# Kernel tuning notes

Hardware: AMD Instinct MI355X
Metric: run time of the kernel (lower is better)

The kernel has to match this reference:

```python
import jax, jax.numpy as jnp
import numpy as np

B = 128
NHEAD = 16
D_MODEL = 512
D_IN = 256  # each of f_* and f_*_out; concat -> 512
N_ATOM = 128


def _scopes():
    lens = np.array([96 + (i % 33) for i in range(B)], dtype=np.int64)  # max == 128 == N_ATOM
    starts_a = np.concatenate([[1], 1 + np.cumsum(lens)[:-1]]).astype(np.int64)
    nb = 2 * lens
    starts_b = np.concatenate([[1], 1 + np.cumsum(nb)[:-1]]).astype(np.int64)
    return lens, starts_a, nb, starts_b


def setup_inputs() -> dict:
    key = jax.random.key(0)
    ks = jax.random.split(key, 10)
    lens, starts_a, nb, starts_b = _scopes()
    Na = int(1 + lens.sum())   # 14279 (row 0 is padding)
    Nb = int(1 + nb.sum())     # 28557 (bond 0 is padding)
    f_atoms = jax.random.normal(ks[0], (Na, D_IN), jnp.float32)
    f_bonds = jax.random.normal(ks[1], (Nb, D_IN), jnp.float32)
    f_atoms_out = jax.random.normal(ks[2], (Na, D_IN), jnp.float32)
    f_bonds_out = jax.random.normal(ks[3], (Nb, D_IN), jnp.float32)
    b2a = jax.random.randint(ks[4], (Nb,), 0, 96, jnp.int64 if jax.config.jax_enable_x64 else jnp.int32)
    b2revb = jax.random.randint(ks[5], (Nb,), 0, Nb, b2a.dtype)
    a_scope = jnp.stack([jnp.asarray(starts_a), jnp.asarray(lens)], axis=1)
    b_scope = jnp.stack([jnp.asarray(starts_b), jnp.asarray(nb)], axis=1)
    W_atom = jax.random.normal(ks[6], (2 * D_IN, D_MODEL), jnp.float32) * 0.02
    b_atom = jnp.zeros((D_MODEL,), jnp.float32)
    W_bond = jax.random.normal(ks[7], (2 * D_IN, NHEAD), jnp.float32) * 0.02
    b_bond = jnp.zeros((NHEAD,), jnp.float32)
    return {"f_atoms": f_atoms, "f_bonds": f_bonds, "f_atoms_out": f_atoms_out,
            "f_bonds_out": f_bonds_out, "b2a": b2a, "b2revb": b2revb,
            "a_scope": a_scope, "b_scope": b_scope, "n_atom": N_ATOM,
            "W_atom": W_atom, "b_atom": b_atom, "W_bond": W_bond, "b_bond": b_bond}


def reference(f_atoms, f_bonds, f_atoms_out, f_bonds_out, b2a, b2revb,
              a_scope, b_scope, n_atom, W_atom, b_atom, W_bond, b_bond):
    Bsz = a_scope.shape[0]
    # atom embedding: concat + linear, drop padding row 0, pad per-molecule -> [n_atom, B, d]
    atoms = jnp.concatenate([f_atoms, f_atoms_out], axis=1) @ W_atom + b_atom  # [Na, d]
    starts_a, lens_a = a_scope[:, 0], a_scope[:, 1]
    pos = jnp.arange(n_atom)
    valid = pos[None, :] < lens_a[:, None]                       # [B, n_atom]
    gidx = jnp.where(valid, starts_a[:, None] + pos[None, :], 0)  # safe gather idx
    atoms_pad = jnp.where(valid[..., None], atoms[gidx], 0.0)     # [B, n_atom, d]
    atoms_emb = atoms_pad.transpose(1, 0, 2)                      # [n_atom, B, d] (batch_first=False)
    # bond embedding -> scatter into dense pairwise matrix
    bonds = jnp.concatenate([f_bonds, f_bonds_out], axis=1) @ W_bond + b_bond  # [Nb, nhead]
    Nb = bonds.shape[0]
    starts_b = b_scope[:, 0]
    mol = jnp.searchsorted(starts_b, jnp.arange(Nb), side='right') - 1  # molecule id per bond (-1 for pad bond 0)
    offset = jnp.maximum(mol, 0) * (n_atom * n_atom)
    idx = b2a + b2a[b2revb] * n_atom + offset                     # flat index into [B*n_atom*n_atom]
    flat = jnp.zeros((Bsz * n_atom * n_atom, bonds.shape[1]), bonds.dtype).at[idx].set(bonds)
    apairs = flat.reshape(Bsz, n_atom, n_atom, -1)                # [B, n_atom, n_atom, nhead]
    padding_mask = ~valid                                         # [B, n_atom], True = pad
    apairs = jnp.where(padding_mask[:, None, :, None], -jnp.inf, apairs)
    apairs = apairs.transpose(0, 3, 1, 2)                         # [B, nhead, n_atom, n_atom]
    return atoms_emb, apairs, padding_mask
```

## Files before the change

### kernel.cpp

```cpp
#include <hip/hip_runtime.h>
#include <math.h>

#define NEG_BIG (-1e30f)

typedef __attribute__((ext_vector_type(8))) short short8;
typedef __attribute__((ext_vector_type(8))) _Float16 half8;
typedef __attribute__((ext_vector_type(4))) float floatx4;

__device__ __forceinline__ unsigned short f2bf(float x) {
    unsigned u = __float_as_uint(x);
    unsigned r = (u + 0x7fffu + ((u >> 16) & 1u)) >> 16;
    return (unsigned short)r;
}
__device__ __forceinline__ short f2h(float x) {
    _Float16 h = (_Float16)x;
    return __builtin_bit_cast(short, h);
}
__device__ __forceinline__ float h2f(short s) {
    return (float)__builtin_bit_cast(_Float16, s);
}


__device__ __forceinline__ void bonds_body(
    int bbid, char* smem,
    const float* __restrict__ fB, const float* __restrict__ fBo,
    const float* __restrict__ Wb_raw, const float* __restrict__ bb_,
    float* __restrict__ bonds, int Nb)
{
    short* feat = (short*)smem;
    short* wb   = (short*)(smem + 17408);

    const int tid = threadIdx.x;
    const int j0 = bbid * 64;

    for (int c = tid; c < 8192; c += 256) {
        int k = c >> 4, h = c & 15;
        wb[h * 512 + ((((k >> 3) + h) & 63) << 3) + (k & 7)] = (short)f2bf(Wb_raw[c]);
    }

    const int wid = tid >> 6, lane = tid & 63;
    const int quad = lane >> 4, l16 = lane & 15;
    floatx4 acc = (floatx4){0.f, 0.f, 0.f, 0.f};

    const int fr = tid >> 2;
    const int fs = (tid & 3) * 32;
    const int j = j0 + fr;

    for (int k0 = 0; k0 < 512; k0 += 128) {
        float x[32];
        if (j < Nb) {
            const float* p = (k0 < 256) ? (fB + (size_t)j * 256 + k0 + fs)
                                        : (fBo + (size_t)j * 256 + (k0 - 256) + fs);
#pragma unroll
            for (int i = 0; i < 8; i++) {
                float4 v = ((const float4*)p)[i];
                x[i * 4 + 0] = v.x; x[i * 4 + 1] = v.y;
                x[i * 4 + 2] = v.z; x[i * 4 + 3] = v.w;
            }
        } else {
#pragma unroll
            for (int i = 0; i < 32; i++) x[i] = 0.f;
        }
        __syncthreads();
#pragma unroll
        for (int c = 0; c < 4; c++) {
            short8 s;
#pragma unroll
            for (int i = 0; i < 8; i++) s[i] = (short)f2bf(x[c * 8 + i]);
            *(short8*)&feat[fr * 136 + fs + c * 8] = s;
        }
        __syncthreads();
#pragma unroll
        for (int kk = 0; kk < 4; kk++) {
            short8 a = *(const short8*)&feat[(wid * 16 + l16) * 136 + kk * 32 + quad * 8];
            int kchunk = (k0 + kk * 32 + quad * 8) >> 3;
            short8 b = *(const short8*)&wb[l16 * 512 + (((kchunk + l16) & 63) * 8)];
            acc = __builtin_amdgcn_mfma_f32_16x16x32_bf16(a, b, acc, 0, 0, 0);
        }
    }
    float bv = bb_[l16];
#pragma unroll
    for (int r = 0; r < 4; r++) {
        int jj = j0 + wid * 16 + quad * 4 + r;
        if (jj < Nb) bonds[(size_t)jj * 16 + l16] = acc[r] + bv;
    }
}

__device__ __forceinline__ void scatter_body(
    int sbid, char* smem,
    const int* __restrict__ b2a, const int* __restrict__ b2revb,
    const int* __restrict__ b_scope, int* __restrict__ winner,
    int Nb, int Bmol)
{
    int* sb = (int*)smem;
    int tid = threadIdx.x;
    if (tid < Bmol) sb[tid] = b_scope[2 * tid];
    __syncthreads();
    int j = sbid * 256 + tid;
    if (j >= Nb) return;
    int lo = 0, hi = Bmol;
    while (lo < hi) { int mid = (lo + hi) >> 1; if (sb[mid] <= j) lo = mid + 1; else hi = mid; }
    int mol = lo - 1; if (mol < 0) mol = 0;
    int p2 = b2a[j];
    int p1 = b2a[b2revb[j]];
    atomicMax(&winner[mol * 16384 + p1 * 128 + p2], j);
}

__device__ __forceinline__ void atoms_body(
    int abid, char* smem,
    const float* __restrict__ fA, const float* __restrict__ fAo,
    const int* __restrict__ a_scope,
    const short* __restrict__ WH, const short* __restrict__ WL,
    const float* __restrict__ bias, float* __restrict__ out, int Bmol)
{
    short* A_s = (short*)smem;
    short* B_s = (short*)(smem + 20480);
    int*   rs  = (int*)(smem + 40960);

    const int tid = threadIdx.x;
    const int n0 = (abid & 3) * 128;
    const int mol = abid >> 2;

    if (tid < 128) {
        int len = a_scope[2 * mol + 1];
        rs[tid] = (tid < len) ? (a_scope[2 * mol] + tid) : -1;
    }
    const int wid = tid >> 6, lane = tid & 63;
    const int wm = (wid >> 1) * 64, wn = (wid & 1) * 64;
    const int quad = lane >> 4, l16 = lane & 15;

    floatx4 acc1[4][4], acc2[4][4];
#pragma unroll
    for (int i = 0; i < 4; i++)
#pragma unroll
        for (int j = 0; j < 4; j++) {
            acc1[i][j] = (floatx4){0.f, 0.f, 0.f, 0.f};
            acc2[i][j] = (floatx4){0.f, 0.f, 0.f, 0.f};
        }

    const int ar = tid >> 1;
    const int ak = (tid & 1) * 16;
    __syncthreads();
    const int asrc = rs[ar];

    for (int k0 = 0; k0 < 512; k0 += 32) {
        float x[16];
        if (asrc >= 0) {
            int kg = k0 + ak;
            const float* p = (kg < 256) ? (fA + (size_t)asrc * 256 + kg)
                                        : (fAo + (size_t)asrc * 256 + (kg - 256));
#pragma unroll
            for (int i = 0; i < 4; i++) {
                float4 v = ((const float4*)p)[i];
                x[i * 4 + 0] = v.x; x[i * 4 + 1] = v.y;
                x[i * 4 + 2] = v.z; x[i * 4 + 3] = v.w;
            }
        } else {
#pragma unroll
            for (int i = 0; i < 16; i++) x[i] = 0.f;
        }
        size_t goff = (size_t)(n0 + ar) * 512 + k0 + ak;
        short8 bh0 = *(const short8*)(WH + goff);
        short8 bh1 = *(const short8*)(WH + goff + 8);
        short8 bl0 = *(const short8*)(WL + goff);
        short8 bl1 = *(const short8*)(WL + goff + 8);

        short8 ah0, ah1, al0, al1;
#pragma unroll
        for (int i = 0; i < 8; i++) {
            short h = f2h(x[i]);
            float r = (x[i] - h2f(h)) * 2048.0f;
            ah0[i] = h; al0[i] = f2h(r);
        }
#pragma unroll
        for (int i = 0; i < 8; i++) {
            float xx = x[8 + i];
            short h = f2h(xx);
            float r = (xx - h2f(h)) * 2048.0f;
            ah1[i] = h; al1[i] = f2h(r);
        }

        __syncthreads();
        const int abase = ar * 40 + ak;
        *(short8*)&A_s[abase] = ah0;          *(short8*)&A_s[abase + 8] = ah1;
        *(short8*)&A_s[5120 + abase] = al0;   *(short8*)&A_s[5120 + abase + 8] = al1;
        *(short8*)&B_s[abase] = bh0;          *(short8*)&B_s[abase + 8] = bh1;
        *(short8*)&B_s[5120 + abase] = bl0;   *(short8*)&B_s[5120 + abase + 8] = bl1;
        __syncthreads();

        half8 afh[4], afl[4];
#pragma unroll
        for (int ti = 0; ti < 4; ti++) {
            int off = (wm + ti * 16 + l16) * 40 + quad * 8;
            afh[ti] = *(const half8*)&A_s[off];
            afl[ti] = *(const half8*)&A_s[5120 + off];
        }
#pragma unroll
        for (int tj = 0; tj < 4; tj++) {
            int off = (wn + tj * 16 + l16) * 40 + quad * 8;
            half8 bh = *(const half8*)&B_s[off];
            half8 bl = *(const half8*)&B_s[5120 + off];
#pragma unroll
            for (int ti = 0; ti < 4; ti++) {
                acc1[ti][tj] = __builtin_amdgcn_mfma_f32_16x16x32_f16(afh[ti], bh, acc1[ti][tj], 0, 0, 0);
                acc2[ti][tj] = __builtin_amdgcn_mfma_f32_16x16x32_f16(afh[ti], bl, acc2[ti][tj], 0, 0, 0);
                acc2[ti][tj] = __builtin_amdgcn_mfma_f32_16x16x32_f16(afl[ti], bh, acc2[ti][tj], 0, 0, 0);
            }
        }
    }

#pragma unroll
    for (int tj = 0; tj < 4; tj++) {
        int n = n0 + wn + tj * 16 + l16;
        float bv = bias[n];
#pragma unroll
        for (int ti = 0; ti < 4; ti++) {
#pragma unroll
            for (int r = 0; r < 4; r++) {
                int pos = wm + ti * 16 + quad * 4 + r;
                bool valid = rs[pos] >= 0;
                float v = valid ? (acc1[ti][tj][r] + 4.8828125e-4f * acc2[ti][tj][r] + bv) : 0.f;
                out[((size_t)pos * Bmol + mol) * 512 + n] = v;
            }
        }
    }
}

__device__ __forceinline__ void apairs_body(
    int chunk, const int* __restrict__ winner, const float* __restrict__ bonds,
    const int* __restrict__ a_scope, float* __restrict__ out_ap)
{
    int t = chunk * 256 + threadIdx.x;
    int b = t >> 12;
    int p1 = (t >> 5) & 127;
    int p2q = t & 31;
    int len = a_scope[2 * b + 1];
    const int4 w = ((const int4*)winner)[t];

    int wi0 = w.x, wi1 = w.y, wi2 = w.z, wi3 = w.w;
    float rows[4][16];
#pragma unroll
    for (int c = 0; c < 16; c++) {
        rows[0][c] = 0.f; rows[1][c] = 0.f; rows[2][c] = 0.f; rows[3][c] = 0.f;
    }
    if (wi0 >= 0) {
        const float4* p = (const float4*)(bonds + (size_t)wi0 * 16);
#pragma unroll
        for (int c = 0; c < 4; c++) {
            float4 v = p[c];
            rows[0][4*c+0] = v.x; rows[0][4*c+1] = v.y; rows[0][4*c+2] = v.z; rows[0][4*c+3] = v.w;
        }
    }
    if (wi1 >= 0) {
        const float4* p = (const float4*)(bonds + (size_t)wi1 * 16);
#pragma unroll
        for (int c = 0; c < 4; c++) {
            float4 v = p[c];
            rows[1][4*c+0] = v.x; rows[1][4*c+1] = v.y; rows[1][4*c+2] = v.z; rows[1][4*c+3] = v.w;
        }
    }
    if (wi2 >= 0) {
        const float4* p = (const float4*)(bonds + (size_t)wi2 * 16);
#pragma unroll
        for (int c = 0; c < 4; c++) {
            float4 v = p[c];
            rows[2][4*c+0] = v.x; rows[2][4*c+1] = v.y; rows[2][4*c+2] = v.z; rows[2][4*c+3] = v.w;
        }
    }
    if (wi3 >= 0) {
        const float4* p = (const float4*)(bonds + (size_t)wi3 * 16);
#pragma unroll
        for (int c = 0; c < 4; c++) {
            float4 v = p[c];
            rows[3][4*c+0] = v.x; rows[3][4*c+1] = v.y; rows[3][4*c+2] = v.z; rows[3][4*c+3] = v.w;
        }
    }

    bool iv0 = (p2q * 4 + 0 >= len);
    bool iv1 = (p2q * 4 + 1 >= len);
    bool iv2 = (p2q * 4 + 2 >= len);
    bool iv3 = (p2q * 4 + 3 >= len);
    float* ob = out_ap + ((size_t)b * 16 * 128 + p1) * 128 + p2q * 4;
#pragma unroll
    for (int h = 0; h < 16; h++) {
        float4 v;
        v.x = iv0 ? NEG_BIG : rows[0][h];
        v.y = iv1 ? NEG_BIG : rows[1][h];
        v.z = iv2 ? NEG_BIG : rows[2][h];
        v.w = iv3 ? NEG_BIG : rows[3][h];
        *(float4*)(ob + (size_t)h * 16384) = v;
    }
}

__global__ __launch_bounds__(256) void k_phase1(
    const float* __restrict__ fB, const float* __restrict__ fBo,
    const float* __restrict__ Wb_raw, const float* __restrict__ b_bond,
    float* __restrict__ bonds_ws, int Nb,
    const float* __restrict__ W, short* __restrict__ WH, short* __restrict__ WL,
    const int* __restrict__ b2a, const int* __restrict__ b2revb,
    const int* __restrict__ b_scope, int* __restrict__ winner,
    const int* __restrict__ a_scope, float* __restrict__ mask_out,
    int Bmol, int nBondsB, int nScatB)
{
    __shared__ char smem[33792];
    int bid = blockIdx.x;
    int tid = threadIdx.x;
    if (bid < nBondsB) {
        bonds_body(bid, smem, fB, fBo, Wb_raw, b_bond, bonds_ws, Nb);
        return;
    }
    bid -= nBondsB;
    if (bid < 1024) {
        int t = bid * 256 + tid;
        int n = t >> 9, k = t & 511;
        float x = W[(size_t)k * 512 + n];
        short h = f2h(x);
        float r = (x - h2f(h)) * 2048.0f;
        WH[t] = h;
        WL[t] = f2h(r);
        return;
    }
    bid -= 1024;
    if (bid < nScatB) {
        scatter_body(bid, smem, b2a, b2revb, b_scope, winner, Nb, Bmol);
        return;
    }
    bid -= nScatB;
    {
        int t = bid * 256 + tid;
        if (t < Bmol * 128) {
            int b = t >> 7, p = t & 127;
            mask_out[t] = (p >= a_scope[2 * b + 1]) ? 1.0f : 0.0f;
        }
    }
}

__global__ __launch_bounds__(256, 2) void k_phase2(
    const float* __restrict__ fA, const float* __restrict__ fAo,
    const int* __restrict__ a_scope,
    const short* __restrict__ WH, const short* __restrict__ WL,
    const float* __restrict__ b_atom,
    const int* __restrict__ winner, const float* __restrict__ bonds_ws,
    float* __restrict__ out_emb, float* __restrict__ out_ap,
    int Bmol)
{
    __shared__ char smem[41472];
    const int bid = blockIdx.x;
    const int s = bid & 3;
    int ai = 0;
#pragma unroll
    for (int r = 0; r < 5; r++) {
        if (r == s) {
            atoms_body(bid, smem, fA, fAo, a_scope, WH, WL, b_atom, out_emb, Bmol);
        } else {
            apairs_body(bid * 4 + ai, winner, bonds_ws, a_scope, out_ap);
            ai++;
        }
    }
}

extern "C" void kernel_launch(void* const* d_in, const int* in_sizes, int n_in,
                              void* d_out, int out_size, void* d_ws, size_t ws_size,
                              hipStream_t stream)
{
    const float* f_atoms     = (const float*)d_in[0];
    const float* f_bonds     = (const float*)d_in[1];
    const float* f_atoms_out = (const float*)d_in[2];
    const float* f_bonds_out = (const float*)d_in[3];
    const int*   b2a         = (const int*)d_in[4];
    const int*   b2revb      = (const int*)d_in[5];
    const int*   a_scope     = (const int*)d_in[6];
    const int*   b_scope     = (const int*)d_in[7];
    const float* W_atom      = (const float*)d_in[9];
    const float* b_atom      = (const float*)d_in[10];
    const float* W_bond      = (const float*)d_in[11];
    const float* b_bond      = (const float*)d_in[12];

    const int Bmol = in_sizes[6] / 2;
    const int Nb   = in_sizes[4];

    char* ws = (char*)d_ws;
    size_t off = 0;
    float* bonds_ws = (float*)(ws + off); off += ((size_t)Nb * 16 * 4 + 255) & ~(size_t)255;
    int*   winner   = (int*)(ws + off);   off += (size_t)Bmol * 16384 * 4;
    short* WH       = (short*)(ws + off); off += 512 * 512 * 2;
    short* WL       = (short*)(ws + off); off += 512 * 512 * 2;

    float* out_emb  = (float*)d_out;
    float* out_ap   = out_emb + (size_t)128 * Bmol * 512;
    float* out_mask = out_ap + (size_t)Bmol * 16 * 128 * 128;

    hipMemsetAsync(winner, 0xFF, (size_t)Bmol * 16384 * 4, stream);

    const int nBondsB = (Nb + 63) / 64;
    const int nScatB  = (Nb + 255) / 256;
    const int nMaskB  = (Bmol * 128 + 255) / 256;
    hipLaunchKernelGGL(k_phase1, dim3(nBondsB + 1024 + nScatB + nMaskB), dim3(256), 0, stream,
                       f_bonds, f_bonds_out, W_bond, b_bond, bonds_ws, Nb,
                       W_atom, WH, WL,
                       b2a, b2revb, b_scope, winner,
                       a_scope, out_mask, Bmol, nBondsB, nScatB);

    hipLaunchKernelGGL(k_phase2, dim3(4 * Bmol), dim3(256), 0, stream,
                       f_atoms, f_atoms_out, a_scope, WH, WL, b_atom,
                       winner, bonds_ws, out_emb, out_ap, Bmol);
}
```

Before: 299.4 us.

## Pre-split atom features into MFMA fragment layout and drop LDS staging in GEMM

Moves the fp32-to-fp16 hi/lo split of atom features into phase 1 and stores both atoms and weights in a per-lane MFMA fragment layout. The atom GEMM then loads fragments directly from global memory with no shared-memory staging or barriers. Phase 2 now launches separate blocks for the GEMM and for apairs instead of interleaving them inside one block. The cost is an extra global round trip for the converted atom tiles (about 32 MB of workspace) and phase-1 blocks that write padded rows.

Result: no change. 297.4 us (-0.7%).

```diff
diff --git a/kernel.cpp b/kernel.cpp
--- a/kernel.cpp
+++ b/kernel.cpp
@@ -107,27 +107,25 @@
 }
 
 __device__ __forceinline__ void atoms_body(
-    int abid, char* smem,
-    const float* __restrict__ fA, const float* __restrict__ fAo,
+    int abid,
     const int* __restrict__ a_scope,
-    const short* __restrict__ WH, const short* __restrict__ WL,
+    const short* __restrict__ AHf, const short* __restrict__ ALf,
+    const short* __restrict__ WHf, const short* __restrict__ WLf,
     const float* __restrict__ bias, float* __restrict__ out, int Bmol)
 {
-    short* A_s = (short*)smem;
-    short* B_s = (short*)(smem + 20480);
-    int*   rs  = (int*)(smem + 40960);
-
     const int tid = threadIdx.x;
+    const int mol = abid >> 2;
     const int n0 = (abid & 3) * 128;
-    const int mol = abid >> 2;
-
-    if (tid < 128) {
-        int len = a_scope[2 * mol + 1];
-        rs[tid] = (tid < len) ? (a_scope[2 * mol] + tid) : -1;
-    }
     const int wid = tid >> 6, lane = tid & 63;
     const int wm = (wid >> 1) * 64, wn = (wid & 1) * 64;
     const int quad = lane >> 4, l16 = lane & 15;
+    const int len = a_scope[2 * mol + 1];
+
+    const int laneoff = quad * 128 + l16 * 8;
+    const short* __restrict__ Ah = AHf + (size_t)mol * 65536 + (wm >> 4) * 8192 + laneoff;
+    const short* __restrict__ Al = ALf + (size_t)mol * 65536 + (wm >> 4) * 8192 + laneoff;
+    const short* __restrict__ Bh = WHf + ((n0 + wn) >> 4) * 8192 + laneoff;
+    const short* __restrict__ Bl = WLf + ((n0 + wn) >> 4) * 8192 + laneoff;
 
     floatx4 acc1[4][4], acc2[4][4];
 #pragma unroll
@@ -138,73 +136,26 @@
             acc2[i][j] = (floatx4){0.f, 0.f, 0.f, 0.f};
         }
 
-    const int ar = tid >> 1;
-    const int ak = (tid & 1) * 16;
-    __syncthreads();
-    const int asrc = rs[ar];
-
     for (int k0 = 0; k0 < 512; k0 += 32) {
-        float x[16];
-        if (asrc >= 0) {
-            int kg = k0 + ak;
-            const float* p = (kg < 256) ? (fA + (size_t)asrc * 256 + kg)
-                                        : (fAo + (size_t)asrc * 256 + (kg - 256));
-#pragma unroll
-            for (int i = 0; i < 4; i++) {
-                float4 v = ((const float4*)p)[i];
-                x[i * 4 + 0] = v.x; x[i * 4 + 1] = v.y;
-                x[i * 4 + 2] = v.z; x[i * 4 + 3] = v.w;
-            }
-        } else {
-#pragma unroll
-            for (int i = 0; i < 16; i++) x[i] = 0.f;
-        }
-        size_t goff = (size_t)(n0 + ar) * 512 + k0 + ak;
-        short8 bh0 = *(const short8*)(WH + goff);
-        short8 bh1 = *(const short8*)(WH + goff + 8);
-        short8 bl0 = *(const short8*)(WL + goff);
-        short8 bl1 = *(const short8*)(WL + goff + 8);
-
-        short8 ah0, ah1, al0, al1;
-#pragma unroll
-        for (int i = 0; i < 8; i++) {
-            short h = f2h(x[i]);
-            float r = (x[i] - h2f(h)) * 2048.0f;
-            ah0[i] = h; al0[i] = f2h(r);
-        }
-#pragma unroll
-        for (int i = 0; i < 8; i++) {
-            float xx = x[8 + i];
-            short h = f2h(xx);
-            float r = (xx - h2f(h)) * 2048.0f;
-            ah1[i] = h; al1[i] = f2h(r);
-        }
-
-        __syncthreads();
-        const int abase = ar * 40 + ak;
-        *(short8*)&A_s[abase] = ah0;          *(short8*)&A_s[abase + 8] = ah1;
-        *(short8*)&A_s[5120 + abase] = al0;   *(short8*)&A_s[5120 + abase + 8] = al1;
-        *(short8*)&B_s[abase] = bh0;          *(short8*)&B_s[abase + 8] = bh1;
-        *(short8*)&B_s[5120 + abase] = bl0;   *(short8*)&B_s[5120 + abase + 8] = bl1;
-        __syncthreads();
-
-        half8 afh[4], afl[4];
+        const int koff = k0 * 16;
+        half8 ah[4], al[4], bh[4], bl[4];
 #pragma unroll
         for (int ti = 0; ti < 4; ti++) {
-            int off = (wm + ti * 16 + l16) * 40 + quad * 8;
-            afh[ti] = *(const half8*)&A_s[off];
-            afl[ti] = *(const half8*)&A_s[5120 + off];
+            ah[ti] = *(const half8*)(Ah + ti * 8192 + koff);
+            al[ti] = *(const half8*)(Al + ti * 8192 + koff);
         }
 #pragma unroll
         for (int tj = 0; tj < 4; tj++) {
-            int off = (wn + tj * 16 + l16) * 40 + quad * 8;
-            half8 bh = *(const half8*)&B_s[off];
-            half8 bl = *(const half8*)&B_s[5120 + off];
+            bh[tj] = *(const half8*)(Bh + tj * 8192 + koff);
+            bl[tj] = *(const half8*)(Bl + tj * 8192 + koff);
+        }
+#pragma unroll
+        for (int tj = 0; tj < 4; tj++) {
 #pragma unroll
             for (int ti = 0; ti < 4; ti++) {
-                acc1[ti][tj] = __builtin_amdgcn_mfma_f32_16x16x32_f16(afh[ti], bh, acc1[ti][tj], 0, 0, 0);
-                acc2[ti][tj] = __builtin_amdgcn_mfma_f32_16x16x32_f16(afh[ti], bl, acc2[ti][tj], 0, 0, 0);
-                acc2[ti][tj] = __builtin_amdgcn_mfma_f32_16x16x32_f16(afl[ti], bh, acc2[ti][tj], 0, 0, 0);
+                acc1[ti][tj] = __builtin_amdgcn_mfma_f32_16x16x32_f16(ah[ti], bh[tj], acc1[ti][tj], 0, 0, 0);
+                acc2[ti][tj] = __builtin_amdgcn_mfma_f32_16x16x32_f16(ah[ti], bl[tj], acc2[ti][tj], 0, 0, 0);
+                acc2[ti][tj] = __builtin_amdgcn_mfma_f32_16x16x32_f16(al[ti], bh[tj], acc2[ti][tj], 0, 0, 0);
             }
         }
     }
@@ -218,7 +169,7 @@
 #pragma unroll
             for (int r = 0; r < 4; r++) {
                 int pos = wm + ti * 16 + quad * 4 + r;
-                bool valid = rs[pos] >= 0;
+                bool valid = pos < len;
                 float v = valid ? (acc1[ti][tj][r] + 4.8828125e-4f * acc2[ti][tj][r] + bv) : 0.f;
                 out[((size_t)pos * Bmol + mol) * 512 + n] = v;
             }
@@ -296,7 +247,9 @@
     const float* __restrict__ fB, const float* __restrict__ fBo,
     const float* __restrict__ Wb_raw, const float* __restrict__ b_bond,
     float* __restrict__ bonds_ws, int Nb,
-    const float* __restrict__ W, short* __restrict__ WH, short* __restrict__ WL,
+    const float* __restrict__ fA, const float* __restrict__ fAo,
+    short* __restrict__ AHf, short* __restrict__ ALf,
+    const float* __restrict__ W, short* __restrict__ WHf, short* __restrict__ WLf,
     const int* __restrict__ b2a, const int* __restrict__ b2revb,
     const int* __restrict__ b_scope, int* __restrict__ winner,
     const int* __restrict__ a_scope, float* __restrict__ mask_out,
@@ -310,17 +263,51 @@
         return;
     }
     bid -= nBondsB;
-    if (bid < 1024) {
+    if (bid < 4096) {
         int t = bid * 256 + tid;
-        int n = t >> 9, k = t & 511;
-        float x = W[(size_t)k * 512 + n];
-        short h = f2h(x);
-        float r = (x - h2f(h)) * 2048.0f;
-        WH[t] = h;
-        WL[t] = f2h(r);
-        return;
-    }
-    bid -= 1024;
+        int l16 = t & 15, kq = (t >> 4) & 63, rt = (t >> 10) & 7, mol = t >> 13;
+        int start = a_scope[2 * mol], len = a_scope[2 * mol + 1];
+        int row = rt * 16 + l16;
+        short8 h8, l8;
+#pragma unroll
+        for (int e = 0; e < 8; e++) { h8[e] = 0; l8[e] = 0; }
+        if (row < len) {
+            int kg = kq * 8;
+            const float* p = (kg < 256) ? (fA + (size_t)(start + row) * 256 + kg)
+                                        : (fAo + (size_t)(start + row) * 256 + (kg - 256));
+            float4 v0 = ((const float4*)p)[0];
+            float4 v1 = ((const float4*)p)[1];
+            float xs[8] = {v0.x, v0.y, v0.z, v0.w, v1.x, v1.y, v1.z, v1.w};
+#pragma unroll
+            for (int e = 0; e < 8; e++) {
+                short h = f2h(xs[e]);
+                float r = (xs[e] - h2f(h)) * 2048.0f;
+                h8[e] = h; l8[e] = f2h(r);
+            }
+        }
+        size_t o = (size_t)mol * 65536 + (size_t)(rt * 64 + kq) * 128 + l16 * 8;
+        *(short8*)(AHf + o) = h8;
+        *(short8*)(ALf + o) = l8;
+        return;
+    }
+    bid -= 4096;
+    if (bid < 128) {
+        int t = bid * 256 + tid;
+        int l16 = t & 15, kq = (t >> 4) & 63, nt = t >> 10;
+        short8 h8, l8;
+#pragma unroll
+        for (int e = 0; e < 8; e++) {
+            float x = W[(size_t)(kq * 8 + e) * 512 + nt * 16 + l16];
+            short h = f2h(x);
+            float r = (x - h2f(h)) * 2048.0f;
+            h8[e] = h; l8[e] = f2h(r);
+        }
+        int o = (nt * 64 + kq) * 128 + l16 * 8;
+        *(short8*)(WHf + o) = h8;
+        *(short8*)(WLf + o) = l8;
+        return;
+    }
+    bid -= 128;
     if (bid < nScatB) {
         scatter_body(bid, smem, b2a, b2revb, b_scope, winner, Nb, Bmol);
         return;
@@ -336,27 +323,20 @@
 }
 
 __global__ __launch_bounds__(256, 2) void k_phase2(
-    const float* __restrict__ fA, const float* __restrict__ fAo,
     const int* __restrict__ a_scope,
-    const short* __restrict__ WH, const short* __restrict__ WL,
+    const short* __restrict__ AHf, const short* __restrict__ ALf,
+    const short* __restrict__ WHf, const short* __restrict__ WLf,
     const float* __restrict__ b_atom,
     const int* __restrict__ winner, const float* __restrict__ bonds_ws,
     float* __restrict__ out_emb, float* __restrict__ out_ap,
-    int Bmol)
-{
-    __shared__ char smem[41472];
-    const int bid = blockIdx.x;
-    const int s = bid & 3;
-    int ai = 0;
-#pragma unroll
-    for (int r = 0; r < 5; r++) {
-        if (r == s) {
-            atoms_body(bid, smem, fA, fAo, a_scope, WH, WL, b_atom, out_emb, Bmol);
-        } else {
-            apairs_body(bid * 4 + ai, winner, bonds_ws, a_scope, out_ap);
-            ai++;
-        }
-    }
+    int Bmol, int nAtomsB)
+{
+    int bid = blockIdx.x;
+    if (bid < nAtomsB) {
+        atoms_body(bid, a_scope, AHf, ALf, WHf, WLf, b_atom, out_emb, Bmol);
+        return;
+    }
+    apairs_body(bid - nAtomsB, winner, bonds_ws, a_scope, out_ap);
 }
 
 extern "C" void kernel_launch(void* const* d_in, const int* in_sizes, int n_in,
@@ -383,8 +363,10 @@
     size_t off = 0;
     float* bonds_ws = (float*)(ws + off); off += ((size_t)Nb * 16 * 4 + 255) & ~(size_t)255;
     int*   winner   = (int*)(ws + off);   off += (size_t)Bmol * 16384 * 4;
-    short* WH       = (short*)(ws + off); off += 512 * 512 * 2;
-    short* WL       = (short*)(ws + off); off += 512 * 512 * 2;
+    short* WHf      = (short*)(ws + off); off += 512 * 512 * 2;
+    short* WLf      = (short*)(ws + off); off += 512 * 512 * 2;
+    short* AHf      = (short*)(ws + off); off += (size_t)Bmol * 65536 * 2;
+    short* ALf      = (short*)(ws + off); off += (size_t)Bmol * 65536 * 2;
 
     float* out_emb  = (float*)d_out;
     float* out_ap   = out_emb + (size_t)128 * Bmol * 512;
@@ -395,13 +377,16 @@
     const int nBondsB = (Nb + 63) / 64;
     const int nScatB  = (Nb + 255) / 256;
     const int nMaskB  = (Bmol * 128 + 255) / 256;
-    hipLaunchKernelGGL(k_phase1, dim3(nBondsB + 1024 + nScatB + nMaskB), dim3(256), 0, stream,
+    hipLaunchKernelGGL(k_phase1, dim3(nBondsB + 4096 + 128 + nScatB + nMaskB), dim3(256), 0, stream,
                        f_bonds, f_bonds_out, W_bond, b_bond, bonds_ws, Nb,
-                       W_atom, WH, WL,
+                       f_atoms, f_atoms_out, AHf, ALf,
+                       W_atom, WHf, WLf,
                        b2a, b2revb, b_scope, winner,
                        a_scope, out_mask, Bmol, nBondsB, nScatB);
 
-    hipLaunchKernelGGL(k_phase2, dim3(4 * Bmol), dim3(256), 0, stream,
-                       f_atoms, f_atoms_out, a_scope, WH, WL, b_atom,
-                       winner, bonds_ws, out_emb, out_ap, Bmol);
-}
+    const int nAtomsB = 4 * Bmol;
+    const int nApB    = Bmol * 4096 / 256;
+    hipLaunchKernelGGL(k_phase2, dim3(nAtomsB + nApB), dim3(256), 0, stream,
+                       a_scope, AHf, ALf, WHf, WLf, b_atom,
+                       winner, bonds_ws, out_emb, out_ap, Bmol, nAtomsB);
+}
```
